# Performance work log

Measured on AMD Instinct MI355X. Metric: run time of the kernel, lower is better.

## Reference

```python
import jax, jax.numpy as jnp
import numpy as np

B, H, HKV, D = 64, 32, 8, 128          # batch(seqs), q heads, kv heads, head dim
PAGE, PAGES_PER_SEQ, NUM_PAGES = 32, 64, 4096
SMAX = PAGES_PER_SEQ * PAGE            # 2048 max context tokens
SCALE = 0.08838834764831843            # 1/sqrt(head_dim)


def setup_inputs() -> dict:
    key = jax.random.key(0)
    ks = jax.random.split(key, 8)
    q = jax.random.normal(ks[0], (B, H, D), jnp.float32)
    k = jax.random.normal(ks[1], (B, HKV, D), jnp.float32)
    v = jax.random.normal(ks[2], (B, HKV, D), jnp.float32)
    k_cache = jax.random.normal(ks[3], (NUM_PAGES, PAGE, HKV, D), jnp.float32)
    v_cache = jax.random.normal(ks[4], (NUM_PAGES, PAGE, HKV, D), jnp.float32)
    block_tables = jax.random.randint(ks[5], (B, PAGES_PER_SEQ), 0, NUM_PAGES, jnp.int32)
    context_lens = jax.random.randint(ks[6], (B,), 1, SMAX + 1, jnp.int32)
    slot_mapping = jax.random.randint(ks[7], (B,), 0, NUM_PAGES * PAGE, jnp.int32)
    return {"q": q, "k": k, "v": v, "k_cache": k_cache, "v_cache": v_cache,
            "block_tables": block_tables, "context_lens": context_lens,
            "slot_mapping": slot_mapping}


def reference(q, k, v, k_cache, v_cache, block_tables, context_lens, slot_mapping):
    # --- store_kvcache: scatter new per-token k/v into flat slot space ---
    kc = k_cache.reshape(-1, HKV, D).at[slot_mapping].set(k)
    vc = v_cache.reshape(-1, HKV, D).at[slot_mapping].set(v)
    kc = kc.reshape(NUM_PAGES, PAGE, HKV, D)
    vc = vc.reshape(NUM_PAGES, PAGE, HKV, D)

    # --- paged decode: gather pages per sequence via block tables ---
    gk = kc[block_tables].reshape(B, SMAX, HKV, D)  # [B, S, HKV, D]
    gv = vc[block_tables].reshape(B, SMAX, HKV, D)

    # --- GQA attention: group q heads over kv heads (repeat_interleave) ---
    G = H // HKV
    qg = q.reshape(B, HKV, G, D)
    scores = jnp.einsum('bkgd,bskd->bkgs', qg, gk) * SCALE  # [B, HKV, G, S]
    valid = jnp.arange(SMAX)[None, :] < context_lens[:, None]  # [B, S]
    scores = jnp.where(valid[:, None, None, :], scores, -jnp.inf)
    p = jax.nn.softmax(scores, axis=-1)
    out = jnp.einsum('bkgs,bskd->bkgd', p, gv).reshape(B, H, D)
    return out
```

## Files before the change

kernel.cpp:

```cpp
#include <hip/hip_runtime.h>

#define NB 64
#define NH 32
#define NKV 8
#define HD 128
#define NG 4
#define PAGE 32
#define PPS 64
#define SMAX 2048
#define CHUNK 256
#define NCH (SMAX / CHUNK)
#define SCALE 0.08838834764831843f

__global__ __launch_bounds__(256) void paged_attn_split(
    const float* __restrict__ q,
    const float* __restrict__ knew,
    const float* __restrict__ vnew,
    const float* __restrict__ kcache,
    const float* __restrict__ vcache,
    const int*  __restrict__ btab,
    const int*  __restrict__ ctxlen,
    const int*  __restrict__ slotmap,
    float* __restrict__ pacc,
    float* __restrict__ pml)
{
    const int kh  = blockIdx.x;
    const int b   = blockIdx.y;
    const int c   = blockIdx.z;
    const int tid = threadIdx.x;

    const int S  = ctxlen[b];
    const int c0 = c * CHUNK;
    if (c0 >= S) return;
    const int send = min(S, c0 + CHUNK);

    __shared__ int   bt_s[CHUNK / PAGE];
    __shared__ int   slot_s[NB];
    __shared__ short ovr_s[CHUNK];
    __shared__ float acc_s[8][NG][HD];
    __shared__ float ml_s[8][NG][2];

    if (tid < CHUNK / PAGE) bt_s[tid]  = btab[b * PPS + c * (CHUNK / PAGE) + tid];
    if (tid >= 64 && tid < 128) slot_s[tid - 64] = slotmap[tid - 64];
    __syncthreads();
    {
        const int target = bt_s[tid >> 5] * PAGE + (tid & 31);
        short ov = -1;
        for (int j = 0; j < NB; ++j)
            if (slot_s[j] == target) ov = (short)j;
        ovr_s[tid] = ov;
    }
    __syncthreads();

    const int hw = tid >> 5;
    const int ln = tid & 31;

    const float* qb = q + ((size_t)(b * NH + kh * NG)) * HD + 4 * ln;
    const float4 q0 = *(const float4*)(qb + 0 * HD);
    const float4 q1 = *(const float4*)(qb + 1 * HD);
    const float4 q2 = *(const float4*)(qb + 2 * HD);
    const float4 q3 = *(const float4*)(qb + 3 * HD);

    float m0 = -INFINITY, m1 = -INFINITY, m2 = -INFINITY, m3 = -INFINITY;
    float l0 = 0.f, l1 = 0.f, l2 = 0.f, l3 = 0.f;
    float4 a0 = {0,0,0,0}, a1 = {0,0,0,0}, a2 = {0,0,0,0}, a3 = {0,0,0,0};

    for (int s = c0 + hw; s < send; s += 8) {
        const int r  = s - c0;
        const int ov = ovr_s[r];
        const float* kp;
        const float* vp;
        if (ov >= 0) {
            const size_t o = ((size_t)ov * NKV + kh) * HD + 4 * ln;
            kp = knew + o;
            vp = vnew + o;
        } else {
            const size_t o = (((size_t)bt_s[r >> 5] * PAGE + (r & 31)) * NKV + kh) * HD + 4 * ln;
            kp = kcache + o;
            vp = vcache + o;
        }
        const float4 kv = *(const float4*)kp;
        const float4 vv = *(const float4*)vp;

        float d0 = q0.x * kv.x + q0.y * kv.y + q0.z * kv.z + q0.w * kv.w;
        float d1 = q1.x * kv.x + q1.y * kv.y + q1.z * kv.z + q1.w * kv.w;
        float d2 = q2.x * kv.x + q2.y * kv.y + q2.z * kv.z + q2.w * kv.w;
        float d3 = q3.x * kv.x + q3.y * kv.y + q3.z * kv.z + q3.w * kv.w;

        #pragma unroll
        for (int mk = 1; mk <= 16; mk <<= 1) {
            d0 += __shfl_xor(d0, mk);
            d1 += __shfl_xor(d1, mk);
            d2 += __shfl_xor(d2, mk);
            d3 += __shfl_xor(d3, mk);
        }
        d0 *= SCALE; d1 *= SCALE; d2 *= SCALE; d3 *= SCALE;

        const float n0 = fmaxf(m0, d0), n1 = fmaxf(m1, d1);
        const float n2 = fmaxf(m2, d2), n3 = fmaxf(m3, d3);
        const float e0 = __expf(m0 - n0), e1 = __expf(m1 - n1);
        const float e2 = __expf(m2 - n2), e3 = __expf(m3 - n3);
        const float p0 = __expf(d0 - n0), p1 = __expf(d1 - n1);
        const float p2 = __expf(d2 - n2), p3 = __expf(d3 - n3);
        m0 = n0; m1 = n1; m2 = n2; m3 = n3;
        l0 = l0 * e0 + p0; l1 = l1 * e1 + p1;
        l2 = l2 * e2 + p2; l3 = l3 * e3 + p3;

        a0.x = a0.x * e0 + p0 * vv.x; a0.y = a0.y * e0 + p0 * vv.y;
        a0.z = a0.z * e0 + p0 * vv.z; a0.w = a0.w * e0 + p0 * vv.w;
        a1.x = a1.x * e1 + p1 * vv.x; a1.y = a1.y * e1 + p1 * vv.y;
        a1.z = a1.z * e1 + p1 * vv.z; a1.w = a1.w * e1 + p1 * vv.w;
        a2.x = a2.x * e2 + p2 * vv.x; a2.y = a2.y * e2 + p2 * vv.y;
        a2.z = a2.z * e2 + p2 * vv.z; a2.w = a2.w * e2 + p2 * vv.w;
        a3.x = a3.x * e3 + p3 * vv.x; a3.y = a3.y * e3 + p3 * vv.y;
        a3.z = a3.z * e3 + p3 * vv.z; a3.w = a3.w * e3 + p3 * vv.w;
    }

    *(float4*)&acc_s[hw][0][4 * ln] = a0;
    *(float4*)&acc_s[hw][1][4 * ln] = a1;
    *(float4*)&acc_s[hw][2][4 * ln] = a2;
    *(float4*)&acc_s[hw][3][4 * ln] = a3;
    if (ln == 0) {
        ml_s[hw][0][0] = m0; ml_s[hw][0][1] = l0;
        ml_s[hw][1][0] = m1; ml_s[hw][1][1] = l1;
        ml_s[hw][2][0] = m2; ml_s[hw][2][1] = l2;
        ml_s[hw][3][0] = m3; ml_s[hw][3][1] = l3;
    }
    __syncthreads();

    for (int o = tid; o < NG * HD; o += 256) {
        const int h = o >> 7;
        const int d = o & 127;
        float M = -INFINITY;
        #pragma unroll
        for (int w = 0; w < 8; ++w) M = fmaxf(M, ml_s[w][h][0]);
        float L = 0.f, val = 0.f;
        #pragma unroll
        for (int w = 0; w < 8; ++w) {
            const float mm = ml_s[w][h][0];
            const float sc = (mm == -INFINITY) ? 0.f : __expf(mm - M);
            L   += sc * ml_s[w][h][1];
            val += sc * acc_s[w][h][d];
        }
        const size_t idx = ((size_t)((b * NKV + kh) * NCH + c) * NG + h);
        pacc[idx * HD + d] = val;
        if (d == 0) { pml[idx * 2] = M; pml[idx * 2 + 1] = L; }
    }
}

__global__ __launch_bounds__(256) void paged_attn_combine(
    const int*  __restrict__ ctxlen,
    const float* __restrict__ pacc,
    const float* __restrict__ pml,
    float* __restrict__ out)
{
    const int kh  = blockIdx.x;
    const int b   = blockIdx.y;
    const int tid = threadIdx.x;
    const int S   = ctxlen[b];
    const int nch = (S + CHUNK - 1) / CHUNK;

    __shared__ float ml_s[NCH][NG][2];
    if (tid < nch * NG) {
        const int cc = tid / NG, h = tid % NG;
        const size_t idx = ((size_t)((b * NKV + kh) * NCH + cc) * NG + h);
        ml_s[cc][h][0] = pml[idx * 2];
        ml_s[cc][h][1] = pml[idx * 2 + 1];
    }
    __syncthreads();

    for (int o = tid; o < NG * HD; o += 256) {
        const int h = o >> 7;
        const int d = o & 127;
        float M = -INFINITY;
        for (int cc = 0; cc < nch; ++cc) M = fmaxf(M, ml_s[cc][h][0]);
        float L = 0.f, val = 0.f;
        for (int cc = 0; cc < nch; ++cc) {
            const float sc = __expf(ml_s[cc][h][0] - M);
            L   += sc * ml_s[cc][h][1];
            val += sc * pacc[((size_t)((b * NKV + kh) * NCH + cc) * NG + h) * HD + d];
        }
        out[((size_t)(b * NH + kh * NG + h)) * HD + d] = val / L;
    }
}

__global__ __launch_bounds__(256) void paged_attn_mono(
    const float* __restrict__ q, const float* __restrict__ knew,
    const float* __restrict__ vnew, const float* __restrict__ kcache,
    const float* __restrict__ vcache, const int* __restrict__ btab,
    const int* __restrict__ ctxlen, const int* __restrict__ slotmap,
    float* __restrict__ out)
{
    const int kh  = blockIdx.x;
    const int b   = blockIdx.y;
    const int tid = threadIdx.x;

    __shared__ int   bt_s[PPS];
    __shared__ int   slot_s[NB];
    __shared__ short ovr_s[SMAX];
    __shared__ float acc_s[8][NG][HD];
    __shared__ float ml_s[8][NG][2];

    if (tid < PPS)              bt_s[tid]        = btab[b * PPS + tid];
    if (tid >= 64 && tid < 128) slot_s[tid - 64] = slotmap[tid - 64];
    for (int i = tid; i < SMAX; i += 256) ovr_s[i] = -1;
    __syncthreads();
    if (tid < PPS) {
        const int page = bt_s[tid];
        for (int j = 0; j < NB; ++j) {
            const int slot = slot_s[j];
            if ((slot >> 5) == page) ovr_s[tid * PAGE + (slot & 31)] = (short)j;
        }
    }
    __syncthreads();

    const int S  = ctxlen[b];
    const int hw = tid >> 5;
    const int ln = tid & 31;

    const float* qb = q + ((size_t)(b * NH + kh * NG)) * HD + 4 * ln;
    const float4 q0 = *(const float4*)(qb + 0 * HD);
    const float4 q1 = *(const float4*)(qb + 1 * HD);
    const float4 q2 = *(const float4*)(qb + 2 * HD);
    const float4 q3 = *(const float4*)(qb + 3 * HD);

    float m0 = -INFINITY, m1 = -INFINITY, m2 = -INFINITY, m3 = -INFINITY;
    float l0 = 0.f, l1 = 0.f, l2 = 0.f, l3 = 0.f;
    float4 a0 = {0,0,0,0}, a1 = {0,0,0,0}, a2 = {0,0,0,0}, a3 = {0,0,0,0};

    for (int s = hw; s < S; s += 8) {
        const int ov = ovr_s[s];
        const float* kp; const float* vp;
        if (ov >= 0) {
            const size_t o = ((size_t)ov * NKV + kh) * HD + 4 * ln;
            kp = knew + o; vp = vnew + o;
        } else {
            const size_t o = (((size_t)bt_s[s >> 5] * PAGE + (s & 31)) * NKV + kh) * HD + 4 * ln;
            kp = kcache + o; vp = vcache + o;
        }
        const float4 kv = *(const float4*)kp;
        const float4 vv = *(const float4*)vp;

        float d0 = q0.x * kv.x + q0.y * kv.y + q0.z * kv.z + q0.w * kv.w;
        float d1 = q1.x * kv.x + q1.y * kv.y + q1.z * kv.z + q1.w * kv.w;
        float d2 = q2.x * kv.x + q2.y * kv.y + q2.z * kv.z + q2.w * kv.w;
        float d3 = q3.x * kv.x + q3.y * kv.y + q3.z * kv.z + q3.w * kv.w;
        #pragma unroll
        for (int mk = 1; mk <= 16; mk <<= 1) {
            d0 += __shfl_xor(d0, mk); d1 += __shfl_xor(d1, mk);
            d2 += __shfl_xor(d2, mk); d3 += __shfl_xor(d3, mk);
        }
        d0 *= SCALE; d1 *= SCALE; d2 *= SCALE; d3 *= SCALE;
        const float n0 = fmaxf(m0, d0), n1 = fmaxf(m1, d1);
        const float n2 = fmaxf(m2, d2), n3 = fmaxf(m3, d3);
        const float e0 = __expf(m0 - n0), e1 = __expf(m1 - n1);
        const float e2 = __expf(m2 - n2), e3 = __expf(m3 - n3);
        const float p0 = __expf(d0 - n0), p1 = __expf(d1 - n1);
        const float p2 = __expf(d2 - n2), p3 = __expf(d3 - n3);
        m0 = n0; m1 = n1; m2 = n2; m3 = n3;
        l0 = l0 * e0 + p0; l1 = l1 * e1 + p1;
        l2 = l2 * e2 + p2; l3 = l3 * e3 + p3;
        a0.x = a0.x * e0 + p0 * vv.x; a0.y = a0.y * e0 + p0 * vv.y;
        a0.z = a0.z * e0 + p0 * vv.z; a0.w = a0.w * e0 + p0 * vv.w;
        a1.x = a1.x * e1 + p1 * vv.x; a1.y = a1.y * e1 + p1 * vv.y;
        a1.z = a1.z * e1 + p1 * vv.z; a1.w = a1.w * e1 + p1 * vv.w;
        a2.x = a2.x * e2 + p2 * vv.x; a2.y = a2.y * e2 + p2 * vv.y;
        a2.z = a2.z * e2 + p2 * vv.z; a2.w = a2.w * e2 + p2 * vv.w;
        a3.x = a3.x * e3 + p3 * vv.x; a3.y = a3.y * e3 + p3 * vv.y;
        a3.z = a3.z * e3 + p3 * vv.z; a3.w = a3.w * e3 + p3 * vv.w;
    }

    *(float4*)&acc_s[hw][0][4 * ln] = a0;
    *(float4*)&acc_s[hw][1][4 * ln] = a1;
    *(float4*)&acc_s[hw][2][4 * ln] = a2;
    *(float4*)&acc_s[hw][3][4 * ln] = a3;
    if (ln == 0) {
        ml_s[hw][0][0] = m0; ml_s[hw][0][1] = l0;
        ml_s[hw][1][0] = m1; ml_s[hw][1][1] = l1;
        ml_s[hw][2][0] = m2; ml_s[hw][2][1] = l2;
        ml_s[hw][3][0] = m3; ml_s[hw][3][1] = l3;
    }
    __syncthreads();
    for (int o = tid; o < NG * HD; o += 256) {
        const int h = o >> 7, d = o & 127;
        float M = -INFINITY;
        #pragma unroll
        for (int w = 0; w < 8; ++w) M = fmaxf(M, ml_s[w][h][0]);
        float L = 0.f, val = 0.f;
        #pragma unroll
        for (int w = 0; w < 8; ++w) {
            const float mm = ml_s[w][h][0];
            const float sc = (mm == -INFINITY) ? 0.f : __expf(mm - M);
            L += sc * ml_s[w][h][1];
            val += sc * acc_s[w][h][d];
        }
        out[((size_t)(b * NH + kh * NG + h)) * HD + d] = val / L;
    }
}

extern "C" void kernel_launch(void* const* d_in, const int* in_sizes, int n_in,
                              void* d_out, int out_size, void* d_ws, size_t ws_size,
                              hipStream_t stream) {
    const float* q  = (const float*)d_in[0];
    const float* k  = (const float*)d_in[1];
    const float* v  = (const float*)d_in[2];
    const float* kc = (const float*)d_in[3];
    const float* vc = (const float*)d_in[4];
    const int* bt   = (const int*)d_in[5];
    const int* cl   = (const int*)d_in[6];
    const int* sm   = (const int*)d_in[7];
    float* out = (float*)d_out;

    const size_t nidx = (size_t)NB * NKV * NCH * NG;
    const size_t need = nidx * (HD + 2) * sizeof(float);

    if (ws_size >= need) {
        float* pacc = (float*)d_ws;
        float* pml  = pacc + nidx * HD;
        dim3 gs(NKV, NB, NCH);
        paged_attn_split<<<gs, 256, 0, stream>>>(q, k, v, kc, vc, bt, cl, sm, pacc, pml);
        dim3 gc(NKV, NB);
        paged_attn_combine<<<gc, 256, 0, stream>>>(cl, pacc, pml, out);
    } else {
        dim3 g(NKV, NB);
        paged_attn_mono<<<g, 256, 0, stream>>>(q, k, v, kc, vc, bt, cl, sm, out);
    }
}
```

Before: 110.4 us.

## Use DPP reductions, lazy softmax rescale, and 2-way unrolled KV loads

Replaces the shfl_xor butterfly with DPP row operations plus a ds_swizzle for the 32-lane dot-product reduction. Adds a lazy online-softmax update that skips the rescale exponentials when no running max increases. Unrolls the split kernel's token loop by two so each wave keeps two K/V loads in flight. This targets shuffle latency and exp cost in a memory-latency-bound decode loop, at the price of more registers and a divergent branch.

```diff
diff --git a/kernel.cpp b/kernel.cpp
--- a/kernel.cpp
+++ b/kernel.cpp
@@ -12,245 +12,28 @@
 #define NCH (SMAX / CHUNK)
 #define SCALE 0.08838834764831843f
 
-__global__ __launch_bounds__(256) void paged_attn_split(
-    const float* __restrict__ q,
-    const float* __restrict__ knew,
-    const float* __restrict__ vnew,
-    const float* __restrict__ kcache,
-    const float* __restrict__ vcache,
-    const int*  __restrict__ btab,
-    const int*  __restrict__ ctxlen,
-    const int*  __restrict__ slotmap,
-    float* __restrict__ pacc,
-    float* __restrict__ pml)
+template <int CTRL>
+__device__ __forceinline__ float dpp_xadd(float v) {
+    int t = __builtin_amdgcn_update_dpp(0, __float_as_int(v), CTRL, 0xF, 0xF, false);
+    return v + __int_as_float(t);
+}
+
+__device__ __forceinline__ float rsum32(float x) {
+    x = dpp_xadd<0xB1>(x);
+    x = dpp_xadd<0x4E>(x);
+    x = dpp_xadd<0x124>(x);
+    x = dpp_xadd<0x128>(x);
+    int y = __builtin_amdgcn_ds_swizzle(__float_as_int(x), 0x401F);
+    return x + __int_as_float(y);
+}
+
+__device__ __forceinline__ void oupd(
+    float d0, float d1, float d2, float d3, const float4 vv,
+    float& m0, float& m1, float& m2, float& m3,
+    float& l0, float& l1, float& l2, float& l3,
+    float4& a0, float4& a1, float4& a2, float4& a3)
 {
-    const int kh  = blockIdx.x;
-    const int b   = blockIdx.y;
-    const int c   = blockIdx.z;
-    const int tid = threadIdx.x;
-
-    const int S  = ctxlen[b];
-    const int c0 = c * CHUNK;
-    if (c0 >= S) return;
-    const int send = min(S, c0 + CHUNK);
-
-    __shared__ int   bt_s[CHUNK / PAGE];
-    __shared__ int   slot_s[NB];
-    __shared__ short ovr_s[CHUNK];
-    __shared__ float acc_s[8][NG][HD];
-    __shared__ float ml_s[8][NG][2];
-
-    if (tid < CHUNK / PAGE) bt_s[tid]  = btab[b * PPS + c * (CHUNK / PAGE) + tid];
-    if (tid >= 64 && tid < 128) slot_s[tid - 64] = slotmap[tid - 64];
-    __syncthreads();
-    {
-        const int target = bt_s[tid >> 5] * PAGE + (tid & 31);
-        short ov = -1;
-        for (int j = 0; j < NB; ++j)
-            if (slot_s[j] == target) ov = (short)j;
-        ovr_s[tid] = ov;
-    }
-    __syncthreads();
-
-    const int hw = tid >> 5;
-    const int ln = tid & 31;
-
-    const float* qb = q + ((size_t)(b * NH + kh * NG)) * HD + 4 * ln;
-    const float4 q0 = *(const float4*)(qb + 0 * HD);
-    const float4 q1 = *(const float4*)(qb + 1 * HD);
-    const float4 q2 = *(const float4*)(qb + 2 * HD);
-    const float4 q3 = *(const float4*)(qb + 3 * HD);
-
-    float m0 = -INFINITY, m1 = -INFINITY, m2 = -INFINITY, m3 = -INFINITY;
-    float l0 = 0.f, l1 = 0.f, l2 = 0.f, l3 = 0.f;
-    float4 a0 = {0,0,0,0}, a1 = {0,0,0,0}, a2 = {0,0,0,0}, a3 = {0,0,0,0};
-
-    for (int s = c0 + hw; s < send; s += 8) {
-        const int r  = s - c0;
-        const int ov = ovr_s[r];
-        const float* kp;
-        const float* vp;
-        if (ov >= 0) {
-            const size_t o = ((size_t)ov * NKV + kh) * HD + 4 * ln;
-            kp = knew + o;
-            vp = vnew + o;
-        } else {
-            const size_t o = (((size_t)bt_s[r >> 5] * PAGE + (r & 31)) * NKV + kh) * HD + 4 * ln;
-            kp = kcache + o;
-            vp = vcache + o;
-        }
-        const float4 kv = *(const float4*)kp;
-        const float4 vv = *(const float4*)vp;
-
-        float d0 = q0.x * kv.x + q0.y * kv.y + q0.z * kv.z + q0.w * kv.w;
-        float d1 = q1.x * kv.x + q1.y * kv.y + q1.z * kv.z + q1.w * kv.w;
-        float d2 = q2.x * kv.x + q2.y * kv.y + q2.z * kv.z + q2.w * kv.w;
-        float d3 = q3.x * kv.x + q3.y * kv.y + q3.z * kv.z + q3.w * kv.w;
-
-        #pragma unroll
-        for (int mk = 1; mk <= 16; mk <<= 1) {
-            d0 += __shfl_xor(d0, mk);
-            d1 += __shfl_xor(d1, mk);
-            d2 += __shfl_xor(d2, mk);
-            d3 += __shfl_xor(d3, mk);
-        }
-        d0 *= SCALE; d1 *= SCALE; d2 *= SCALE; d3 *= SCALE;
-
-        const float n0 = fmaxf(m0, d0), n1 = fmaxf(m1, d1);
-        const float n2 = fmaxf(m2, d2), n3 = fmaxf(m3, d3);
-        const float e0 = __expf(m0 - n0), e1 = __expf(m1 - n1);
-        const float e2 = __expf(m2 - n2), e3 = __expf(m3 - n3);
-        const float p0 = __expf(d0 - n0), p1 = __expf(d1 - n1);
-        const float p2 = __expf(d2 - n2), p3 = __expf(d3 - n3);
-        m0 = n0; m1 = n1; m2 = n2; m3 = n3;
-        l0 = l0 * e0 + p0; l1 = l1 * e1 + p1;
-        l2 = l2 * e2 + p2; l3 = l3 * e3 + p3;
-
-        a0.x = a0.x * e0 + p0 * vv.x; a0.y = a0.y * e0 + p0 * vv.y;
-        a0.z = a0.z * e0 + p0 * vv.z; a0.w = a0.w * e0 + p0 * vv.w;
-        a1.x = a1.x * e1 + p1 * vv.x; a1.y = a1.y * e1 + p1 * vv.y;
-        a1.z = a1.z * e1 + p1 * vv.z; a1.w = a1.w * e1 + p1 * vv.w;
-        a2.x = a2.x * e2 + p2 * vv.x; a2.y = a2.y * e2 + p2 * vv.y;
-        a2.z = a2.z * e2 + p2 * vv.z; a2.w = a2.w * e2 + p2 * vv.w;
-        a3.x = a3.x * e3 + p3 * vv.x; a3.y = a3.y * e3 + p3 * vv.y;
-        a3.z = a3.z * e3 + p3 * vv.z; a3.w = a3.w * e3 + p3 * vv.w;
-    }
-
-    *(float4*)&acc_s[hw][0][4 * ln] = a0;
-    *(float4*)&acc_s[hw][1][4 * ln] = a1;
-    *(float4*)&acc_s[hw][2][4 * ln] = a2;
-    *(float4*)&acc_s[hw][3][4 * ln] = a3;
-    if (ln == 0) {
-        ml_s[hw][0][0] = m0; ml_s[hw][0][1] = l0;
-        ml_s[hw][1][0] = m1; ml_s[hw][1][1] = l1;
-        ml_s[hw][2][0] = m2; ml_s[hw][2][1] = l2;
-        ml_s[hw][3][0] = m3; ml_s[hw][3][1] = l3;
-    }
-    __syncthreads();
-
-    for (int o = tid; o < NG * HD; o += 256) {
-        const int h = o >> 7;
-        const int d = o & 127;
-        float M = -INFINITY;
-        #pragma unroll
-        for (int w = 0; w < 8; ++w) M = fmaxf(M, ml_s[w][h][0]);
-        float L = 0.f, val = 0.f;
-        #pragma unroll
-        for (int w = 0; w < 8; ++w) {
-            const float mm = ml_s[w][h][0];
-            const float sc = (mm == -INFINITY) ? 0.f : __expf(mm - M);
-            L   += sc * ml_s[w][h][1];
-            val += sc * acc_s[w][h][d];
-        }
-        const size_t idx = ((size_t)((b * NKV + kh) * NCH + c) * NG + h);
-        pacc[idx * HD + d] = val;
-        if (d == 0) { pml[idx * 2] = M; pml[idx * 2 + 1] = L; }
-    }
-}
-
-__global__ __launch_bounds__(256) void paged_attn_combine(
-    const int*  __restrict__ ctxlen,
-    const float* __restrict__ pacc,
-    const float* __restrict__ pml,
-    float* __restrict__ out)
-{
-    const int kh  = blockIdx.x;
-    const int b   = blockIdx.y;
-    const int tid = threadIdx.x;
-    const int S   = ctxlen[b];
-    const int nch = (S + CHUNK - 1) / CHUNK;
-
-    __shared__ float ml_s[NCH][NG][2];
-    if (tid < nch * NG) {
-        const int cc = tid / NG, h = tid % NG;
-        const size_t idx = ((size_t)((b * NKV + kh) * NCH + cc) * NG + h);
-        ml_s[cc][h][0] = pml[idx * 2];
-        ml_s[cc][h][1] = pml[idx * 2 + 1];
-    }
-    __syncthreads();
-
-    for (int o = tid; o < NG * HD; o += 256) {
-        const int h = o >> 7;
-        const int d = o & 127;
-        float M = -INFINITY;
-        for (int cc = 0; cc < nch; ++cc) M = fmaxf(M, ml_s[cc][h][0]);
-        float L = 0.f, val = 0.f;
-        for (int cc = 0; cc < nch; ++cc) {
-            const float sc = __expf(ml_s[cc][h][0] - M);
-            L   += sc * ml_s[cc][h][1];
-            val += sc * pacc[((size_t)((b * NKV + kh) * NCH + cc) * NG + h) * HD + d];
-        }
-        out[((size_t)(b * NH + kh * NG + h)) * HD + d] = val / L;
-    }
-}
-
-__global__ __launch_bounds__(256) void paged_attn_mono(
-    const float* __restrict__ q, const float* __restrict__ knew,
-    const float* __restrict__ vnew, const float* __restrict__ kcache,
-    const float* __restrict__ vcache, const int* __restrict__ btab,
-    const int* __restrict__ ctxlen, const int* __restrict__ slotmap,
-    float* __restrict__ out)
-{
-    const int kh  = blockIdx.x;
-    const int b   = blockIdx.y;
-    const int tid = threadIdx.x;
-
-    __shared__ int   bt_s[PPS];
-    __shared__ int   slot_s[NB];
-    __shared__ short ovr_s[SMAX];
-    __shared__ float acc_s[8][NG][HD];
-    __shared__ float ml_s[8][NG][2];
-
-    if (tid < PPS)              bt_s[tid]        = btab[b * PPS + tid];
-    if (tid >= 64 && tid < 128) slot_s[tid - 64] = slotmap[tid - 64];
-    for (int i = tid; i < SMAX; i += 256) ovr_s[i] = -1;
-    __syncthreads();
-    if (tid < PPS) {
-        const int page = bt_s[tid];
-        for (int j = 0; j < NB; ++j) {
-            const int slot = slot_s[j];
-            if ((slot >> 5) == page) ovr_s[tid * PAGE + (slot & 31)] = (short)j;
-        }
-    }
-    __syncthreads();
-
-    const int S  = ctxlen[b];
-    const int hw = tid >> 5;
-    const int ln = tid & 31;
-
-    const float* qb = q + ((size_t)(b * NH + kh * NG)) * HD + 4 * ln;
-    const float4 q0 = *(const float4*)(qb + 0 * HD);
-    const float4 q1 = *(const float4*)(qb + 1 * HD);
-    const float4 q2 = *(const float4*)(qb + 2 * HD);
-    const float4 q3 = *(const float4*)(qb + 3 * HD);
-
-    float m0 = -INFINITY, m1 = -INFINITY, m2 = -INFINITY, m3 = -INFINITY;
-    float l0 = 0.f, l1 = 0.f, l2 = 0.f, l3 = 0.f;
-    float4 a0 = {0,0,0,0}, a1 = {0,0,0,0}, a2 = {0,0,0,0}, a3 = {0,0,0,0};
-
-    for (int s = hw; s < S; s += 8) {
-        const int ov = ovr_s[s];
-        const float* kp; const float* vp;
-        if (ov >= 0) {
-            const size_t o = ((size_t)ov * NKV + kh) * HD + 4 * ln;
-            kp = knew + o; vp = vnew + o;
-        } else {
-            const size_t o = (((size_t)bt_s[s >> 5] * PAGE + (s & 31)) * NKV + kh) * HD + 4 * ln;
-            kp = kcache + o; vp = vcache + o;
-        }
-        const float4 kv = *(const float4*)kp;
-        const float4 vv = *(const float4*)vp;
-
-        float d0 = q0.x * kv.x + q0.y * kv.y + q0.z * kv.z + q0.w * kv.w;
-        float d1 = q1.x * kv.x + q1.y * kv.y + q1.z * kv.z + q1.w * kv.w;
-        float d2 = q2.x * kv.x + q2.y * kv.y + q2.z * kv.z + q2.w * kv.w;
-        float d3 = q3.x * kv.x + q3.y * kv.y + q3.z * kv.z + q3.w * kv.w;
-        #pragma unroll
-        for (int mk = 1; mk <= 16; mk <<= 1) {
-            d0 += __shfl_xor(d0, mk); d1 += __shfl_xor(d1, mk);
-            d2 += __shfl_xor(d2, mk); d3 += __shfl_xor(d3, mk);
-        }
-        d0 *= SCALE; d1 *= SCALE; d2 *= SCALE; d3 *= SCALE;
+    if (d0 > m0 || d1 > m1 || d2 > m2 || d3 > m3) {
         const float n0 = fmaxf(m0, d0), n1 = fmaxf(m1, d1);
         const float n2 = fmaxf(m2, d2), n3 = fmaxf(m3, d3);
         const float e0 = __expf(m0 - n0), e1 = __expf(m1 - n1);
@@ -268,6 +51,254 @@
         a2.z = a2.z * e2 + p2 * vv.z; a2.w = a2.w * e2 + p2 * vv.w;
         a3.x = a3.x * e3 + p3 * vv.x; a3.y = a3.y * e3 + p3 * vv.y;
         a3.z = a3.z * e3 + p3 * vv.z; a3.w = a3.w * e3 + p3 * vv.w;
+    } else {
+        const float p0 = __expf(d0 - m0), p1 = __expf(d1 - m1);
+        const float p2 = __expf(d2 - m2), p3 = __expf(d3 - m3);
+        l0 += p0; l1 += p1; l2 += p2; l3 += p3;
+        a0.x += p0 * vv.x; a0.y += p0 * vv.y; a0.z += p0 * vv.z; a0.w += p0 * vv.w;
+        a1.x += p1 * vv.x; a1.y += p1 * vv.y; a1.z += p1 * vv.z; a1.w += p1 * vv.w;
+        a2.x += p2 * vv.x; a2.y += p2 * vv.y; a2.z += p2 * vv.z; a2.w += p2 * vv.w;
+        a3.x += p3 * vv.x; a3.y += p3 * vv.y; a3.z += p3 * vv.z; a3.w += p3 * vv.w;
+    }
+}
+
+__global__ __launch_bounds__(256) void paged_attn_split(
+    const float* __restrict__ q,
+    const float* __restrict__ knew,
+    const float* __restrict__ vnew,
+    const float* __restrict__ kcache,
+    const float* __restrict__ vcache,
+    const int*  __restrict__ btab,
+    const int*  __restrict__ ctxlen,
+    const int*  __restrict__ slotmap,
+    float* __restrict__ pacc,
+    float* __restrict__ pml)
+{
+    const int kh  = blockIdx.x;
+    const int b   = blockIdx.y;
+    const int c   = blockIdx.z;
+    const int tid = threadIdx.x;
+
+    const int S  = ctxlen[b];
+    const int c0 = c * CHUNK;
+    if (c0 >= S) return;
+    const int send = min(S, c0 + CHUNK);
+
+    __shared__ int   bt_s[CHUNK / PAGE];
+    __shared__ int   slot_s[NB];
+    __shared__ short ovr_s[CHUNK];
+    __shared__ float acc_s[8][NG][HD];
+    __shared__ float ml_s[8][NG][2];
+
+    if (tid < CHUNK / PAGE) bt_s[tid]  = btab[b * PPS + c * (CHUNK / PAGE) + tid];
+    if (tid >= 64 && tid < 128) slot_s[tid - 64] = slotmap[tid - 64];
+    __syncthreads();
+    {
+        const int target = bt_s[tid >> 5] * PAGE + (tid & 31);
+        short ov = -1;
+        for (int j = 0; j < NB; ++j)
+            if (slot_s[j] == target) ov = (short)j;
+        ovr_s[tid] = ov;
+    }
+    __syncthreads();
+
+    const int hw = tid >> 5;
+    const int ln = tid & 31;
+
+    const float* qb = q + ((size_t)(b * NH + kh * NG)) * HD + 4 * ln;
+    const float4 q0 = *(const float4*)(qb + 0 * HD);
+    const float4 q1 = *(const float4*)(qb + 1 * HD);
+    const float4 q2 = *(const float4*)(qb + 2 * HD);
+    const float4 q3 = *(const float4*)(qb + 3 * HD);
+
+    float m0 = -INFINITY, m1 = -INFINITY, m2 = -INFINITY, m3 = -INFINITY;
+    float l0 = 0.f, l1 = 0.f, l2 = 0.f, l3 = 0.f;
+    float4 a0 = {0,0,0,0}, a1 = {0,0,0,0}, a2 = {0,0,0,0}, a3 = {0,0,0,0};
+
+    auto addr = [&](int sg, const float*& kp, const float*& vp) {
+        const int r  = sg - c0;
+        const int ov = ovr_s[r];
+        if (ov >= 0) {
+            const size_t o = ((size_t)ov * NKV + kh) * HD + 4 * ln;
+            kp = knew + o; vp = vnew + o;
+        } else {
+            const size_t o = (((size_t)bt_s[r >> 5] * PAGE + (r & 31)) * NKV + kh) * HD + 4 * ln;
+            kp = kcache + o; vp = vcache + o;
+        }
+    };
+
+    int s = c0 + hw;
+    for (; s + 8 < send; s += 16) {
+        const float *kpA, *vpA, *kpB, *vpB;
+        addr(s,     kpA, vpA);
+        addr(s + 8, kpB, vpB);
+        const float4 kA = *(const float4*)kpA;
+        const float4 kB = *(const float4*)kpB;
+        const float4 vA = *(const float4*)vpA;
+        const float4 vB = *(const float4*)vpB;
+
+        float dA0 = q0.x*kA.x + q0.y*kA.y + q0.z*kA.z + q0.w*kA.w;
+        float dA1 = q1.x*kA.x + q1.y*kA.y + q1.z*kA.z + q1.w*kA.w;
+        float dA2 = q2.x*kA.x + q2.y*kA.y + q2.z*kA.z + q2.w*kA.w;
+        float dA3 = q3.x*kA.x + q3.y*kA.y + q3.z*kA.z + q3.w*kA.w;
+        float dB0 = q0.x*kB.x + q0.y*kB.y + q0.z*kB.z + q0.w*kB.w;
+        float dB1 = q1.x*kB.x + q1.y*kB.y + q1.z*kB.z + q1.w*kB.w;
+        float dB2 = q2.x*kB.x + q2.y*kB.y + q2.z*kB.z + q2.w*kB.w;
+        float dB3 = q3.x*kB.x + q3.y*kB.y + q3.z*kB.z + q3.w*kB.w;
+
+        dA0 = rsum32(dA0) * SCALE; dA1 = rsum32(dA1) * SCALE;
+        dA2 = rsum32(dA2) * SCALE; dA3 = rsum32(dA3) * SCALE;
+        dB0 = rsum32(dB0) * SCALE; dB1 = rsum32(dB1) * SCALE;
+        dB2 = rsum32(dB2) * SCALE; dB3 = rsum32(dB3) * SCALE;
+
+        oupd(dA0, dA1, dA2, dA3, vA, m0,m1,m2,m3, l0,l1,l2,l3, a0,a1,a2,a3);
+        oupd(dB0, dB1, dB2, dB3, vB, m0,m1,m2,m3, l0,l1,l2,l3, a0,a1,a2,a3);
+    }
+    if (s < send) {
+        const float *kp, *vp;
+        addr(s, kp, vp);
+        const float4 kv = *(const float4*)kp;
+        const float4 vv = *(const float4*)vp;
+        float d0 = q0.x*kv.x + q0.y*kv.y + q0.z*kv.z + q0.w*kv.w;
+        float d1 = q1.x*kv.x + q1.y*kv.y + q1.z*kv.z + q1.w*kv.w;
+        float d2 = q2.x*kv.x + q2.y*kv.y + q2.z*kv.z + q2.w*kv.w;
+        float d3 = q3.x*kv.x + q3.y*kv.y + q3.z*kv.z + q3.w*kv.w;
+        d0 = rsum32(d0) * SCALE; d1 = rsum32(d1) * SCALE;
+        d2 = rsum32(d2) * SCALE; d3 = rsum32(d3) * SCALE;
+        oupd(d0, d1, d2, d3, vv, m0,m1,m2,m3, l0,l1,l2,l3, a0,a1,a2,a3);
+    }
+
+    *(float4*)&acc_s[hw][0][4 * ln] = a0;
+    *(float4*)&acc_s[hw][1][4 * ln] = a1;
+    *(float4*)&acc_s[hw][2][4 * ln] = a2;
+    *(float4*)&acc_s[hw][3][4 * ln] = a3;
+    if (ln == 0) {
+        ml_s[hw][0][0] = m0; ml_s[hw][0][1] = l0;
+        ml_s[hw][1][0] = m1; ml_s[hw][1][1] = l1;
+        ml_s[hw][2][0] = m2; ml_s[hw][2][1] = l2;
+        ml_s[hw][3][0] = m3; ml_s[hw][3][1] = l3;
+    }
+    __syncthreads();
+
+    for (int o = tid; o < NG * HD; o += 256) {
+        const int h = o >> 7;
+        const int d = o & 127;
+        float M = -INFINITY;
+        #pragma unroll
+        for (int w = 0; w < 8; ++w) M = fmaxf(M, ml_s[w][h][0]);
+        float L = 0.f, val = 0.f;
+        #pragma unroll
+        for (int w = 0; w < 8; ++w) {
+            const float mm = ml_s[w][h][0];
+            const float sc = (mm == -INFINITY) ? 0.f : __expf(mm - M);
+            L   += sc * ml_s[w][h][1];
+            val += sc * acc_s[w][h][d];
+        }
+        const size_t idx = ((size_t)((b * NKV + kh) * NCH + c) * NG + h);
+        pacc[idx * HD + d] = val;
+        if (d == 0) { pml[idx * 2] = M; pml[idx * 2 + 1] = L; }
+    }
+}
+
+__global__ __launch_bounds__(256) void paged_attn_combine(
+    const int*  __restrict__ ctxlen,
+    const float* __restrict__ pacc,
+    const float* __restrict__ pml,
+    float* __restrict__ out)
+{
+    const int kh  = blockIdx.x;
+    const int b   = blockIdx.y;
+    const int tid = threadIdx.x;
+    const int S   = ctxlen[b];
+    const int nch = (S + CHUNK - 1) / CHUNK;
+
+    __shared__ float ml_s[NCH][NG][2];
+    if (tid < nch * NG) {
+        const int cc = tid / NG, h = tid % NG;
+        const size_t idx = ((size_t)((b * NKV + kh) * NCH + cc) * NG + h);
+        ml_s[cc][h][0] = pml[idx * 2];
+        ml_s[cc][h][1] = pml[idx * 2 + 1];
+    }
+    __syncthreads();
+
+    for (int o = tid; o < NG * HD; o += 256) {
+        const int h = o >> 7;
+        const int d = o & 127;
+        float M = -INFINITY;
+        for (int cc = 0; cc < nch; ++cc) M = fmaxf(M, ml_s[cc][h][0]);
+        float L = 0.f, val = 0.f;
+        for (int cc = 0; cc < nch; ++cc) {
+            const float sc = __expf(ml_s[cc][h][0] - M);
+            L   += sc * ml_s[cc][h][1];
+            val += sc * pacc[((size_t)((b * NKV + kh) * NCH + cc) * NG + h) * HD + d];
+        }
+        out[((size_t)(b * NH + kh * NG + h)) * HD + d] = val / L;
+    }
+}
+
+__global__ __launch_bounds__(256) void paged_attn_mono(
+    const float* __restrict__ q, const float* __restrict__ knew,
+    const float* __restrict__ vnew, const float* __restrict__ kcache,
+    const float* __restrict__ vcache, const int* __restrict__ btab,
+    const int* __restrict__ ctxlen, const int* __restrict__ slotmap,
+    float* __restrict__ out)
+{
+    const int kh  = blockIdx.x;
+    const int b   = blockIdx.y;
+    const int tid = threadIdx.x;
+
+    __shared__ int   bt_s[PPS];
+    __shared__ int   slot_s[NB];
+    __shared__ short ovr_s[SMAX];
+    __shared__ float acc_s[8][NG][HD];
+    __shared__ float ml_s[8][NG][2];
+
+    if (tid < PPS)              bt_s[tid]        = btab[b * PPS + tid];
+    if (tid >= 64 && tid < 128) slot_s[tid - 64] = slotmap[tid - 64];
+    for (int i = tid; i < SMAX; i += 256) ovr_s[i] = -1;
+    __syncthreads();
+    if (tid < PPS) {
+        const int page = bt_s[tid];
+        for (int j = 0; j < NB; ++j) {
+            const int slot = slot_s[j];
+            if ((slot >> 5) == page) ovr_s[tid * PAGE + (slot & 31)] = (short)j;
+        }
+    }
+    __syncthreads();
+
+    const int S  = ctxlen[b];
+    const int hw = tid >> 5;
+    const int ln = tid & 31;
+
+    const float* qb = q + ((size_t)(b * NH + kh * NG)) * HD + 4 * ln;
+    const float4 q0 = *(const float4*)(qb + 0 * HD);
+    const float4 q1 = *(const float4*)(qb + 1 * HD);
+    const float4 q2 = *(const float4*)(qb + 2 * HD);
+    const float4 q3 = *(const float4*)(qb + 3 * HD);
+
+    float m0 = -INFINITY, m1 = -INFINITY, m2 = -INFINITY, m3 = -INFINITY;
+    float l0 = 0.f, l1 = 0.f, l2 = 0.f, l3 = 0.f;
+    float4 a0 = {0,0,0,0}, a1 = {0,0,0,0}, a2 = {0,0,0,0}, a3 = {0,0,0,0};
+
+    for (int s = hw; s < S; s += 8) {
+        const int ov = ovr_s[s];
+        const float* kp; const float* vp;
+        if (ov >= 0) {
+            const size_t o = ((size_t)ov * NKV + kh) * HD + 4 * ln;
+            kp = knew + o; vp = vnew + o;
+        } else {
+            const size_t o = (((size_t)bt_s[s >> 5] * PAGE + (s & 31)) * NKV + kh) * HD + 4 * ln;
+            kp = kcache + o; vp = vcache + o;
+        }
+        const float4 kv = *(const float4*)kp;
+        const float4 vv = *(const float4*)vp;
+        float d0 = q0.x*kv.x + q0.y*kv.y + q0.z*kv.z + q0.w*kv.w;
+        float d1 = q1.x*kv.x + q1.y*kv.y + q1.z*kv.z + q1.w*kv.w;
+        float d2 = q2.x*kv.x + q2.y*kv.y + q2.z*kv.z + q2.w*kv.w;
+        float d3 = q3.x*kv.x + q3.y*kv.y + q3.z*kv.z + q3.w*kv.w;
+        d0 = rsum32(d0) * SCALE; d1 = rsum32(d1) * SCALE;
+        d2 = rsum32(d2) * SCALE; d3 = rsum32(d3) * SCALE;
+        oupd(d0, d1, d2, d3, vv, m0,m1,m2,m3, l0,l1,l2,l3, a0,a1,a2,a3);
     }
 
     *(float4*)&acc_s[hw][0][4 * ln] = a0;
```

After: 107.0 us. -3.0%, faster.
